# Kernel optimization log

Measured on AMD Instinct MI355X. Metric: run time of the kernel, lower is better.

The kernel has to match this reference:

```python
import jax, jax.numpy as jnp
import numpy as np

NUM_LAYERS = 12
D = 256          # d_model
H = 8            # n_head
DK = D // H      # qk_dim = v_dim = 32
FFD = 1024       # ffd_dim
B, L = 32, 448
EPS = 1e-6
MAXLEN = 500


def _sinusoidal_pos_emb(maxlen, hidden_dim):
    depth = hidden_dim / 2
    positions = np.arange(maxlen, dtype=np.float32)[:, None]
    depths = np.arange(depth, dtype=np.float32)[None, :] / depth
    angle_rads = positions * (1.0 / np.power(10000.0, depths))
    pe = np.concatenate([np.sin(angle_rads), np.cos(angle_rads)], axis=-1)
    return jnp.asarray(pe, jnp.float32)


def setup_inputs() -> dict:
    key = jax.random.key(0)
    ks = jax.random.split(key, 16)
    s = 0.02
    inp = {
        "x": jax.random.normal(ks[0], (B, L, D), jnp.float32),
        "mask": jnp.zeros((B, L), jnp.bool_),
        "pos_emb": _sinusoidal_pos_emb(MAXLEN - 1, D)[:L],  # [L, D]
        "Wq": jax.random.normal(ks[1], (NUM_LAYERS, D, D), jnp.float32) * s,
        "bq": jnp.zeros((NUM_LAYERS, D), jnp.float32),
        "Wk": jax.random.normal(ks[2], (NUM_LAYERS, D, D), jnp.float32) * s,
        "bk": jnp.zeros((NUM_LAYERS, D), jnp.float32),
        "Wv": jax.random.normal(ks[3], (NUM_LAYERS, D, D), jnp.float32) * s,
        "bv": jnp.zeros((NUM_LAYERS, D), jnp.float32),
        "Wo": jax.random.normal(ks[4], (NUM_LAYERS, D, D), jnp.float32) * s,
        "bo": jnp.zeros((NUM_LAYERS, D), jnp.float32),
        "W1": jax.random.normal(ks[5], (NUM_LAYERS, D, FFD), jnp.float32) * s,
        "bf1": jnp.zeros((NUM_LAYERS, FFD), jnp.float32),
        "W2": jax.random.normal(ks[6], (NUM_LAYERS, FFD, D), jnp.float32) * s,
        "bf2": jnp.zeros((NUM_LAYERS, D), jnp.float32),
        "ln1_g": jnp.ones((NUM_LAYERS, D), jnp.float32),
        "ln1_b": jnp.zeros((NUM_LAYERS, D), jnp.float32),
        "ln2_g": jnp.ones((NUM_LAYERS, D), jnp.float32),
        "ln2_b": jnp.zeros((NUM_LAYERS, D), jnp.float32),
    }
    return inp


def _layer_norm(x, g, b):
    mu = jnp.mean(x, axis=-1, keepdims=True)
    var = jnp.mean(jnp.square(x - mu), axis=-1, keepdims=True)
    return (x - mu) * jax.lax.rsqrt(var + EPS) * g + b


def _encoder_forward(x, mask, pos_emb, Wq, bq, Wk, bk, Wv, bv, Wo, bo,
                     W1, bf1, W2, bf2, ln1_g, ln1_b, ln2_g, ln2_b):
    Bx, Lx, _ = x.shape
    scale = 1.0 / np.sqrt(DK)
    x = x + pos_emb[None, :Lx, :]
    mask_b = mask[:, None, None, :]  # [B,1,1,L], True = masked
    for i in range(NUM_LAYERS):
        # --- pre-norm attention ---
        nx = _layer_norm(x, ln1_g[i], ln1_b[i])
        q = (nx @ Wq[i] + bq[i]).reshape(Bx, Lx, H, DK)
        k = (nx @ Wk[i] + bk[i]).reshape(Bx, Lx, H, DK)
        v = (nx @ Wv[i] + bv[i]).reshape(Bx, Lx, H, DK)
        dot = jnp.einsum("bihd,bjhd->bhij", q, k) * scale
        dot = jnp.where(mask_b, -10000.0, dot)
        attn = jax.nn.softmax(dot, axis=-1)
        o = jnp.einsum("bhij,bjhd->bihd", attn, v).reshape(Bx, Lx, D)
        x = x + (o @ Wo[i] + bo[i])
        # --- pre-norm FFN (exact GELU, as torch nn.GELU) ---
        nx2 = _layer_norm(x, ln2_g[i], ln2_b[i])
        h = jax.nn.gelu(nx2 @ W1[i] + bf1[i], approximate=False)
        x = x + (h @ W2[i] + bf2[i])
    return x


def reference(x, mask, pos_emb, Wq, bq, Wk, bk, Wv, bv, Wo, bo,
              W1, bf1, W2, bf2, ln1_g, ln1_b, ln2_g, ln2_b):
    return _encoder_forward(x, mask, pos_emb, Wq, bq, Wk, bk, Wv, bv, Wo, bo,
                            W1, bf1, W2, bf2, ln1_g, ln1_b, ln2_g, ln2_b)
```

## Files before the change

kernel.cpp:

```cpp
#include <hip/hip_runtime.h>

#define NL 12
#define DM 256
#define FFDIM 1024
#define BBATCH 32
#define LSEQ 448
#define MTOK (BBATCH*LSEQ)
#define EPSF 1e-6f
#define QSCALE_LOG2E (0.17677669529663687f * 1.4426950408889634f)

typedef __attribute__((ext_vector_type(8))) short bf16x8;
typedef __attribute__((ext_vector_type(4))) float f32x4;
typedef unsigned short u16;
typedef unsigned int u32;

__device__ __forceinline__ u16 f2bf(float f) {
    union { float f; u32 u; } v; v.f = f;
    u32 r = v.u + 0x7fffu + ((v.u >> 16) & 1u);
    return (u16)(r >> 16);
}
__device__ __forceinline__ float gelu_exact(float x) {
    return 0.5f * x * (1.0f + erff(x * 0.70710678118654752f));
}
__device__ __forceinline__ void gload16(const u16* g, u16* l) {
    __builtin_amdgcn_global_load_lds(
        (const __attribute__((address_space(1))) u32*)g,
        (__attribute__((address_space(3))) u32*)l, 16, 0, 0);
}

__global__ __launch_bounds__(256) void add_pos_k(
    const float* __restrict__ x, const float* __restrict__ pe, float* __restrict__ out)
{
    int i = blockIdx.x * 256 + threadIdx.x;
    float4 xv = ((const float4*)x)[i];
    float4 pv = ((const float4*)pe)[i % (LSEQ * DM / 4)];
    float4 r;
    r.x = xv.x + pv.x; r.y = xv.y + pv.y; r.z = xv.z + pv.z; r.w = xv.w + pv.w;
    ((float4*)out)[i] = r;
}

__global__ __launch_bounds__(256) void ln_k(
    const float* __restrict__ x, const float* __restrict__ g,
    const float* __restrict__ b, u16* __restrict__ out)
{
    const int w = threadIdx.x >> 6, lane = threadIdx.x & 63;
    const int row = blockIdx.x * 4 + w;
    float4 v = ((const float4*)(x + (size_t)row * DM))[lane];
    float s = v.x + v.y + v.z + v.w;
#pragma unroll
    for (int off = 32; off; off >>= 1) s += __shfl_xor(s, off);
    float mu = s * (1.0f / 256.0f);
    float d0 = v.x - mu, d1 = v.y - mu, d2 = v.z - mu, d3 = v.w - mu;
    float sq = d0*d0 + d1*d1 + d2*d2 + d3*d3;
#pragma unroll
    for (int off = 32; off; off >>= 1) sq += __shfl_xor(sq, off);
    float rs = rsqrtf(sq * (1.0f / 256.0f) + EPSF);
    float4 gv = ((const float4*)g)[lane];
    float4 bv = ((const float4*)b)[lane];
    ushort4 o;
    o.x = f2bf(d0 * rs * gv.x + bv.x);
    o.y = f2bf(d1 * rs * gv.y + bv.y);
    o.z = f2bf(d2 * rs * gv.z + bv.z);
    o.w = f2bf(d3 * rs * gv.w + bv.w);
    *(ushort4*)(out + (size_t)row * DM + lane * 4) = o;
}

__global__ __launch_bounds__(256) void twt_k(
    const float* __restrict__ in, u16* __restrict__ out,
    int K, int N, int in_lstride, int out_lstride)
{
    __shared__ float tl[32][33];
    const int l = blockIdx.z;
    const int n0 = blockIdx.x * 32, k0 = blockIdx.y * 32;
    const int tx = threadIdx.x & 31, ty = threadIdx.x >> 5;
    const float* src = in + (size_t)l * in_lstride;
#pragma unroll
    for (int i = 0; i < 4; ++i)
        tl[ty + 8*i][tx] = src[(size_t)(k0 + ty + 8*i) * N + n0 + tx];
    __syncthreads();
    u16* dst = out + (size_t)l * out_lstride;
#pragma unroll
    for (int i = 0; i < 4; ++i)
        dst[(size_t)(n0 + ty + 8*i) * K + k0 + tx] = f2bf(tl[tx][ty + 8*i]);
}

__global__ __launch_bounds__(256) void pack_bias_k(
    const float* __restrict__ bq, const float* __restrict__ bk,
    const float* __restrict__ bv, float* __restrict__ bqkv)
{
    int i = blockIdx.x * 256 + threadIdx.x;
    if (i >= NL * 768) return;
    int l = i / 768, c = i % 768;
    float v = (c < 256) ? bq[l*256 + c] : (c < 512) ? bk[l*256 + c - 256] : bv[l*256 + c - 512];
    bqkv[i] = v;
}

template<int BN, int EPI>
__global__ __launch_bounds__(256, (BN == 64) ? 4 : 3) void mm_k(
    const u16* __restrict__ A, int lda, const u16* __restrict__ Bt,
    const float* __restrict__ bias, void* __restrict__ C, int ldc, int K,
    u16* __restrict__ vtg)
{
    __shared__ u16 As[2][128 * 32];
    __shared__ u16 Bs[2][BN * 32];
    constexpr int MT = BN / 32;
    const int tid = threadIdx.x;
    const int by = blockIdx.x, bx = blockIdx.y;
    const int w = tid >> 6, lane = tid & 63;
    const int lm = lane & 15, lk = lane >> 4;
    const int m0 = (BN == 128) ? ((w >> 1) * 64) : (w * 32);
    const int n0 = (BN == 128) ? ((w & 1) * 64) : 0;
    const int lrow = lane >> 2, lcol = (lane & 3) * 8;

    const u16* Ab = A + (size_t)(by * 128) * lda;
    const u16* Bb = Bt + (size_t)(bx * BN) * K;

    f32x4 zz = {0.f, 0.f, 0.f, 0.f};
    f32x4 acc[MT][4];
#pragma unroll
    for (int i = 0; i < MT; ++i)
#pragma unroll
        for (int j = 0; j < 4; ++j) acc[i][j] = zz;

    auto stage = [&](int buf, int k0) {
#pragma unroll
        for (int i = 0; i < 2; ++i) {
            int seg = w * 2 + i;
            gload16(Ab + (size_t)(seg * 16 + lrow) * lda + k0 + lcol, &As[buf][seg * 512]);
        }
        if constexpr (BN == 128) {
#pragma unroll
            for (int i = 0; i < 2; ++i) {
                int seg = w * 2 + i;
                gload16(Bb + (size_t)(seg * 16 + lrow) * K + k0 + lcol, &Bs[buf][seg * 512]);
            }
        } else {
            gload16(Bb + (size_t)(w * 16 + lrow) * K + k0 + lcol, &Bs[buf][w * 512]);
        }
    };

    stage(0, 0);
    const int NK = K >> 5;
    for (int it = 0; it < NK; ++it) {
        const int cur = it & 1;
        __syncthreads();
        if (it + 1 < NK) stage(1 - cur, (it + 1) * 32);
        bf16x8 af[MT], bfr[4];
#pragma unroll
        for (int mt = 0; mt < MT; ++mt)
            af[mt] = *(const bf16x8*)&As[cur][(m0 + mt*16 + lm)*32 + lk*8];
#pragma unroll
        for (int nt = 0; nt < 4; ++nt)
            bfr[nt] = *(const bf16x8*)&Bs[cur][(n0 + nt*16 + lm)*32 + lk*8];
#pragma unroll
        for (int mt = 0; mt < MT; ++mt)
#pragma unroll
            for (int nt = 0; nt < 4; ++nt)
                acc[mt][nt] = __builtin_amdgcn_mfma_f32_16x16x32_bf16(af[mt], bfr[nt], acc[mt][nt], 0, 0, 0);
    }

    float bv[4];
#pragma unroll
    for (int nt = 0; nt < 4; ++nt) bv[nt] = bias[bx*BN + n0 + nt*16 + lm];
#pragma unroll
    for (int mt = 0; mt < MT; ++mt) {
        int grow0 = by*128 + m0 + mt*16 + lk*4;
#pragma unroll
        for (int nt = 0; nt < 4; ++nt) {
            int gcol = bx*BN + n0 + nt*16 + lm;
            float v0 = acc[mt][nt][0] + bv[nt];
            float v1 = acc[mt][nt][1] + bv[nt];
            float v2 = acc[mt][nt][2] + bv[nt];
            float v3 = acc[mt][nt][3] + bv[nt];
            if constexpr (EPI == 1) {
                u16* cp = (u16*)C + (size_t)grow0 * ldc + gcol;
                cp[0]            = f2bf(gelu_exact(v0));
                cp[ldc]          = f2bf(gelu_exact(v1));
                cp[2*(size_t)ldc] = f2bf(gelu_exact(v2));
                cp[3*(size_t)ldc] = f2bf(gelu_exact(v3));
            } else if constexpr (EPI == 3) {
                if (gcol < 512) {
                    float qs = (gcol < 256) ? QSCALE_LOG2E : 1.0f;
                    u16* cp = (u16*)C + (size_t)grow0 * ldc + gcol;
                    cp[0]            = f2bf(v0 * qs);
                    cp[ldc]          = f2bf(v1 * qs);
                    cp[2*(size_t)ldc] = f2bf(v2 * qs);
                    cp[3*(size_t)ldc] = f2bf(v3 * qs);
                } else {
                    int c = gcol - 512;
                    int hh = c >> 5, d = c & 31;
                    u32 bidx = (u32)grow0 / 448u;
                    int srow = grow0 - (int)bidx * 448;
                    ushort4 st;
                    st.x = f2bf(v0); st.y = f2bf(v1); st.z = f2bf(v2); st.w = f2bf(v3);
                    *(ushort4*)&vtg[((size_t)(bidx*8 + hh)*32 + d)*448 + srow] = st;
                }
            } else {
                float* p = (float*)C + (size_t)grow0 * ldc + gcol;
                p[0]   += v0;
                p[ldc] += v1;
                p[2*(size_t)ldc] += v2;
                p[3*(size_t)ldc] += v3;
            }
        }
    }
}

__global__ __launch_bounds__(256, 4) void attn_k(
    const u16* __restrict__ qkv, const u16* __restrict__ vtg,
    const unsigned char* __restrict__ mask, u16* __restrict__ ob)
{
    __shared__ u16 Klds[448 * 32];
    __shared__ u16 Plds[4][16 * 68];
    const int tid = threadIdx.x, w = tid >> 6, lane = tid & 63;
    const int lm = lane & 15, lk = lane >> 4;
    const int bid = blockIdx.x;
    const int bh = bid & 255, sg = bid >> 8;
    const int b = bh >> 3, h = bh & 7;
    const size_t rowbase = (size_t)b * LSEQ;

#pragma unroll
    for (int i = 0; i < 7; ++i) {
        int seg = w * 7 + i;
        gload16(qkv + (rowbase + seg * 16 + (lane >> 2)) * 768 + 256 + h * 32 + (lane & 3) * 8,
                &Klds[seg * 512]);
    }
    unsigned mbits = 0;
#pragma unroll
    for (int t = 0; t < 28; ++t)
        mbits |= (mask[b * LSEQ + t * 16 + lm] ? 1u : 0u) << t;
    __syncthreads();

    const u16* Vb = vtg + (size_t)bh * 32 * 448;
    f32x4 zz = {0.f, 0.f, 0.f, 0.f};

    const int q0 = (sg * 4 + w) * 16;
    bf16x8 qf = *(const bf16x8*)(qkv + (rowbase + q0 + lm) * 768 + h * 32 + lk * 8);

    f32x4 oacc[2] = {zz, zz};
    float sum[4] = {0.f, 0.f, 0.f, 0.f};
    u16* P = &Plds[w][0];
#pragma unroll
    for (int cc = 0; cc < 7; ++cc) {
#pragma unroll
        for (int tt = 0; tt < 4; ++tt) {
            int t = cc*4 + tt;
            bf16x8 kf = *(const bf16x8*)&Klds[(t*16 + lm)*32 + lk*8];
            f32x4 s = __builtin_amdgcn_mfma_f32_16x16x32_bf16(qf, kf, zz, 0, 0, 0);
            bool m = (mbits >> t) & 1;
#pragma unroll
            for (int r = 0; r < 4; ++r) {
                float e = m ? 0.f : exp2f(s[r]);
                sum[r] += e;
                P[(lk*4 + r)*68 + tt*16 + lm] = f2bf(e);
            }
        }
        bf16x8 pa0 = *(const bf16x8*)&P[lm*68 + lk*8];
        bf16x8 pa1 = *(const bf16x8*)&P[lm*68 + 32 + lk*8];
#pragma unroll
        for (int dt = 0; dt < 2; ++dt) {
            bf16x8 vb0 = *(const bf16x8*)(Vb + (size_t)(dt*16 + lm)*448 + cc*64 + lk*8);
            bf16x8 vb1 = *(const bf16x8*)(Vb + (size_t)(dt*16 + lm)*448 + cc*64 + 32 + lk*8);
            oacc[dt] = __builtin_amdgcn_mfma_f32_16x16x32_bf16(pa0, vb0, oacc[dt], 0, 0, 0);
            oacc[dt] = __builtin_amdgcn_mfma_f32_16x16x32_bf16(pa1, vb1, oacc[dt], 0, 0, 0);
        }
    }
#pragma unroll
    for (int off = 1; off < 16; off <<= 1)
#pragma unroll
        for (int r = 0; r < 4; ++r) sum[r] += __shfl_xor(sum[r], off);
    float inv[4];
#pragma unroll
    for (int r = 0; r < 4; ++r) inv[r] = 1.0f / sum[r];

#pragma unroll
    for (int dt = 0; dt < 2; ++dt)
#pragma unroll
        for (int r = 0; r < 4; ++r)
            ob[(rowbase + q0 + lk*4 + r)*256 + h*32 + dt*16 + lm] = f2bf(oacc[dt][r] * inv[r]);
}

extern "C" void kernel_launch(void* const* d_in, const int* in_sizes, int n_in,
                              void* d_out, int out_size, void* d_ws, size_t ws_size,
                              hipStream_t stream)
{
    const float* x_in = (const float*)d_in[0];
    const unsigned char* mask = (const unsigned char*)d_in[1];
    const float* pe   = (const float*)d_in[2];
    const float* Wq = (const float*)d_in[3];
    const float* bq = (const float*)d_in[4];
    const float* Wk = (const float*)d_in[5];
    const float* bk = (const float*)d_in[6];
    const float* Wv = (const float*)d_in[7];
    const float* bv = (const float*)d_in[8];
    const float* Wo = (const float*)d_in[9];
    const float* bo = (const float*)d_in[10];
    const float* W1 = (const float*)d_in[11];
    const float* bf1 = (const float*)d_in[12];
    const float* W2 = (const float*)d_in[13];
    const float* bf2 = (const float*)d_in[14];
    const float* ln1_g = (const float*)d_in[15];
    const float* ln1_b = (const float*)d_in[16];
    const float* ln2_g = (const float*)d_in[17];
    const float* ln2_b = (const float*)d_in[18];

    float* x = (float*)d_out;
    u16* ws = (u16*)d_ws;
    u16* nx   = ws;
    u16* qkv  = nx + 3670016;
    u16* ob   = qkv + 11010048;
    u16* vtg  = ob + 3670016;
    u16* hb   = qkv;
    u16* wqkvt = vtg + 3670016;
    u16* wot  = wqkvt + 2359296;
    u16* w1t  = wot + 786432;
    u16* w2t  = w1t + 3145728;
    float* bqkv = (float*)(w2t + 3145728);

    add_pos_k<<<MTOK * DM / 1024, 256, 0, stream>>>(x_in, pe, x);

    twt_k<<<dim3(8, 8, NL), 256, 0, stream>>>(Wq, wqkvt,          256, 256, 65536, 196608);
    twt_k<<<dim3(8, 8, NL), 256, 0, stream>>>(Wk, wqkvt + 65536,  256, 256, 65536, 196608);
    twt_k<<<dim3(8, 8, NL), 256, 0, stream>>>(Wv, wqkvt + 131072, 256, 256, 65536, 196608);
    twt_k<<<dim3(8, 8, NL), 256, 0, stream>>>(Wo, wot, 256, 256, 65536, 65536);
    twt_k<<<dim3(32, 8, NL), 256, 0, stream>>>(W1, w1t, 256, 1024, 262144, 262144);
    twt_k<<<dim3(8, 32, NL), 256, 0, stream>>>(W2, w2t, 1024, 256, 262144, 262144);
    pack_bias_k<<<(NL * 768 + 255) / 256, 256, 0, stream>>>(bq, bk, bv, bqkv);

    for (int l = 0; l < NL; ++l) {
        ln_k<<<MTOK / 4, 256, 0, stream>>>(x, ln1_g + l*256, ln1_b + l*256, nx);
        mm_k<128, 3><<<dim3(112, 6), 256, 0, stream>>>(
            nx, 256, wqkvt + (size_t)l*196608, bqkv + l*768, qkv, 768, 256, vtg);
        attn_k<<<1792, 256, 0, stream>>>(qkv, vtg, mask, ob);
        mm_k<64, 2><<<dim3(112, 4), 256, 0, stream>>>(
            ob, 256, wot + (size_t)l*65536, bo + l*256, x, 256, 256, nullptr);
        ln_k<<<MTOK / 4, 256, 0, stream>>>(x, ln2_g + l*256, ln2_b + l*256, nx);
        mm_k<128, 1><<<dim3(112, 8), 256, 0, stream>>>(
            nx, 256, w1t + (size_t)l*262144, bf1 + l*1024, hb, 1024, 256, nullptr);
        mm_k<64, 2><<<dim3(112, 4), 256, 0, stream>>>(
            hb, 1024, w2t + (size_t)l*262144, bf2 + l*256, x, 256, 1024, nullptr);
    }
}
```

Measured before the change: 1.541 ms.

## Fuse residual add and LayerNorm into full-row output-projection GEMM epilogues

```diff
diff --git a/kernel.cpp b/kernel.cpp
--- a/kernel.cpp
+++ b/kernel.cpp
@@ -28,24 +28,18 @@
         (__attribute__((address_space(3))) u32*)l, 16, 0, 0);
 }
 
-__global__ __launch_bounds__(256) void add_pos_k(
-    const float* __restrict__ x, const float* __restrict__ pe, float* __restrict__ out)
-{
-    int i = blockIdx.x * 256 + threadIdx.x;
-    float4 xv = ((const float4*)x)[i];
-    float4 pv = ((const float4*)pe)[i % (LSEQ * DM / 4)];
-    float4 r;
-    r.x = xv.x + pv.x; r.y = xv.y + pv.y; r.z = xv.z + pv.z; r.w = xv.w + pv.w;
-    ((float4*)out)[i] = r;
-}
-
-__global__ __launch_bounds__(256) void ln_k(
-    const float* __restrict__ x, const float* __restrict__ g,
-    const float* __restrict__ b, u16* __restrict__ out)
+__global__ __launch_bounds__(256) void ln0_k(
+    const float* __restrict__ xin, const float* __restrict__ pe,
+    const float* __restrict__ g, const float* __restrict__ b,
+    float* __restrict__ x, u16* __restrict__ nx)
 {
     const int w = threadIdx.x >> 6, lane = threadIdx.x & 63;
     const int row = blockIdx.x * 4 + w;
-    float4 v = ((const float4*)(x + (size_t)row * DM))[lane];
+    const int prow = row % LSEQ;
+    float4 v = ((const float4*)(xin + (size_t)row * DM))[lane];
+    float4 p = ((const float4*)(pe + (size_t)prow * DM))[lane];
+    v.x += p.x; v.y += p.y; v.z += p.z; v.w += p.w;
+    ((float4*)(x + (size_t)row * DM))[lane] = v;
     float s = v.x + v.y + v.z + v.w;
 #pragma unroll
     for (int off = 32; off; off >>= 1) s += __shfl_xor(s, off);
@@ -62,7 +56,7 @@
     o.y = f2bf(d1 * rs * gv.y + bv.y);
     o.z = f2bf(d2 * rs * gv.z + bv.z);
     o.w = f2bf(d3 * rs * gv.w + bv.w);
-    *(ushort4*)(out + (size_t)row * DM + lane * 4) = o;
+    *(ushort4*)(nx + (size_t)row * DM + lane * 4) = o;
 }
 
 __global__ __launch_bounds__(256) void twt_k(
@@ -95,95 +89,86 @@
     bqkv[i] = v;
 }
 
-template<int BN, int EPI>
-__global__ __launch_bounds__(256, (BN == 64) ? 4 : 3) void mm_k(
+template<int EPI>
+__global__ __launch_bounds__(256, 3) void mm_k(
     const u16* __restrict__ A, int lda, const u16* __restrict__ Bt,
-    const float* __restrict__ bias, void* __restrict__ C, int ldc, int K,
+    const float* __restrict__ bias, u16* __restrict__ C, int ldc, int K,
     u16* __restrict__ vtg)
 {
     __shared__ u16 As[2][128 * 32];
-    __shared__ u16 Bs[2][BN * 32];
-    constexpr int MT = BN / 32;
+    __shared__ u16 Bs[2][128 * 32];
     const int tid = threadIdx.x;
     const int by = blockIdx.x, bx = blockIdx.y;
     const int w = tid >> 6, lane = tid & 63;
     const int lm = lane & 15, lk = lane >> 4;
-    const int m0 = (BN == 128) ? ((w >> 1) * 64) : (w * 32);
-    const int n0 = (BN == 128) ? ((w & 1) * 64) : 0;
+    const int m0 = (w >> 1) * 64, n0 = (w & 1) * 64;
     const int lrow = lane >> 2, lcol = (lane & 3) * 8;
 
     const u16* Ab = A + (size_t)(by * 128) * lda;
-    const u16* Bb = Bt + (size_t)(bx * BN) * K;
+    const u16* Bb = Bt + (size_t)(bx * 128) * K;
 
     f32x4 zz = {0.f, 0.f, 0.f, 0.f};
-    f32x4 acc[MT][4];
-#pragma unroll
-    for (int i = 0; i < MT; ++i)
+    f32x4 acc[4][4];
+#pragma unroll
+    for (int i = 0; i < 4; ++i)
 #pragma unroll
         for (int j = 0; j < 4; ++j) acc[i][j] = zz;
 
-    auto stage = [&](int buf, int k0) {
-#pragma unroll
-        for (int i = 0; i < 2; ++i) {
-            int seg = w * 2 + i;
-            gload16(Ab + (size_t)(seg * 16 + lrow) * lda + k0 + lcol, &As[buf][seg * 512]);
-        }
-        if constexpr (BN == 128) {
+    for (int k0 = 0; k0 < K; k0 += 64) {
+        __syncthreads();
+#pragma unroll
+        for (int p = 0; p < 2; ++p)
 #pragma unroll
             for (int i = 0; i < 2; ++i) {
                 int seg = w * 2 + i;
-                gload16(Bb + (size_t)(seg * 16 + lrow) * K + k0 + lcol, &Bs[buf][seg * 512]);
-            }
-        } else {
-            gload16(Bb + (size_t)(w * 16 + lrow) * K + k0 + lcol, &Bs[buf][w * 512]);
-        }
-    };
-
-    stage(0, 0);
-    const int NK = K >> 5;
-    for (int it = 0; it < NK; ++it) {
-        const int cur = it & 1;
+                gload16(Ab + (size_t)(seg * 16 + lrow) * lda + k0 + p * 32 + lcol,
+                        &As[p][seg * 512]);
+                gload16(Bb + (size_t)(seg * 16 + lrow) * K + k0 + p * 32 + lcol,
+                        &Bs[p][seg * 512]);
+            }
         __syncthreads();
-        if (it + 1 < NK) stage(1 - cur, (it + 1) * 32);
-        bf16x8 af[MT], bfr[4];
-#pragma unroll
-        for (int mt = 0; mt < MT; ++mt)
-            af[mt] = *(const bf16x8*)&As[cur][(m0 + mt*16 + lm)*32 + lk*8];
-#pragma unroll
-        for (int nt = 0; nt < 4; ++nt)
-            bfr[nt] = *(const bf16x8*)&Bs[cur][(n0 + nt*16 + lm)*32 + lk*8];
-#pragma unroll
-        for (int mt = 0; mt < MT; ++mt)
+#pragma unroll
+        for (int p = 0; p < 2; ++p) {
+            bf16x8 af[4], bfr[4];
+#pragma unroll
+            for (int mt = 0; mt < 4; ++mt)
+                af[mt] = *(const bf16x8*)&As[p][(m0 + mt*16 + lm)*32 + lk*8];
 #pragma unroll
             for (int nt = 0; nt < 4; ++nt)
-                acc[mt][nt] = __builtin_amdgcn_mfma_f32_16x16x32_bf16(af[mt], bfr[nt], acc[mt][nt], 0, 0, 0);
+                bfr[nt] = *(const bf16x8*)&Bs[p][(n0 + nt*16 + lm)*32 + lk*8];
+#pragma unroll
+            for (int mt = 0; mt < 4; ++mt)
+#pragma unroll
+                for (int nt = 0; nt < 4; ++nt)
+                    acc[mt][nt] = __builtin_amdgcn_mfma_f32_16x16x32_bf16(af[mt], bfr[nt], acc[mt][nt], 0, 0, 0);
+        }
     }
 
     float bv[4];
 #pragma unroll
-    for (int nt = 0; nt < 4; ++nt) bv[nt] = bias[bx*BN + n0 + nt*16 + lm];
-#pragma unroll
-    for (int mt = 0; mt < MT; ++mt) {
+    for (int nt = 0; nt < 4; ++nt) bv[nt] = bias[bx*128 + n0 + nt*16 + lm];
+#pragma unroll
+    for (int mt = 0; mt < 4; ++mt) {
         int grow0 = by*128 + m0 + mt*16 + lk*4;
 #pragma unroll
         for (int nt = 0; nt < 4; ++nt) {
-            int gcol = bx*BN + n0 + nt*16 + lm;
+            int gcol = bx*128 + n0 + nt*16 + lm;
             float v0 = acc[mt][nt][0] + bv[nt];
             float v1 = acc[mt][nt][1] + bv[nt];
             float v2 = acc[mt][nt][2] + bv[nt];
             float v3 = acc[mt][nt][3] + bv[nt];
             if constexpr (EPI == 1) {
-                u16* cp = (u16*)C + (size_t)grow0 * ldc + gcol;
-                cp[0]            = f2bf(gelu_exact(v0));
-                cp[ldc]          = f2bf(gelu_exact(v1));
+                u16* cp = C + (size_t)grow0 * ldc + gcol;
+                cp[0]             = f2bf(gelu_exact(v0));
+                cp[ldc]           = f2bf(gelu_exact(v1));
                 cp[2*(size_t)ldc] = f2bf(gelu_exact(v2));
                 cp[3*(size_t)ldc] = f2bf(gelu_exact(v3));
-            } else if constexpr (EPI == 3) {
+            } else {
                 if (gcol < 512) {
                     float qs = (gcol < 256) ? QSCALE_LOG2E : 1.0f;
-                    u16* cp = (u16*)C + (size_t)grow0 * ldc + gcol;
-                    cp[0]            = f2bf(v0 * qs);
-                    cp[ldc]          = f2bf(v1 * qs);
+                    u16* cp = C + (size_t)grow0 * ldc + gcol;
+                    cp[0]             = f2bf(v0 * qs);
+                    cp[ldc]           = f2bf(v1 * qs);
                     cp[2*(size_t)ldc] = f2bf(v2 * qs);
                     cp[3*(size_t)ldc] = f2bf(v3 * qs);
                 } else {
@@ -195,13 +180,111 @@
                     st.x = f2bf(v0); st.y = f2bf(v1); st.z = f2bf(v2); st.w = f2bf(v3);
                     *(ushort4*)&vtg[((size_t)(bidx*8 + hh)*32 + d)*448 + srow] = st;
                 }
-            } else {
-                float* p = (float*)C + (size_t)grow0 * ldc + gcol;
-                p[0]   += v0;
-                p[ldc] += v1;
-                p[2*(size_t)ldc] += v2;
-                p[3*(size_t)ldc] += v3;
-            }
+            }
+        }
+    }
+}
+
+template<bool DOLN>
+__global__ __launch_bounds__(256, 3) void mmrow_k(
+    const u16* __restrict__ A, int lda, const u16* __restrict__ Bt,
+    const float* __restrict__ bias, float* __restrict__ X,
+    const float* __restrict__ g, const float* __restrict__ b,
+    u16* __restrict__ nx, int K)
+{
+    __shared__ u16 As[2][64 * 32];
+    __shared__ u16 Bs[2][256 * 32];
+    const int tid = threadIdx.x, by = blockIdx.x;
+    const int w = tid >> 6, lane = tid & 63;
+    const int lm = lane & 15, lk = lane >> 4;
+    const int m0 = w * 16;
+    const int lrow = lane >> 2, lcol = (lane & 3) * 8;
+
+    const u16* Ab = A + (size_t)(by * 64) * lda;
+
+    f32x4 zz = {0.f, 0.f, 0.f, 0.f};
+    f32x4 acc[16];
+#pragma unroll
+    for (int i = 0; i < 16; ++i) acc[i] = zz;
+
+    for (int k0 = 0; k0 < K; k0 += 64) {
+        __syncthreads();
+#pragma unroll
+        for (int p = 0; p < 2; ++p) {
+            gload16(Ab + (size_t)(w * 16 + lrow) * lda + k0 + p * 32 + lcol,
+                    &As[p][w * 512]);
+#pragma unroll
+            for (int i = 0; i < 4; ++i) {
+                int seg = w * 4 + i;
+                gload16(Bt + (size_t)(seg * 16 + lrow) * K + k0 + p * 32 + lcol,
+                        &Bs[p][seg * 512]);
+            }
+        }
+        __syncthreads();
+#pragma unroll
+        for (int p = 0; p < 2; ++p) {
+            bf16x8 af = *(const bf16x8*)&As[p][(m0 + lm)*32 + lk*8];
+#pragma unroll
+            for (int nt = 0; nt < 16; ++nt) {
+                bf16x8 bfr = *(const bf16x8*)&Bs[p][(nt*16 + lm)*32 + lk*8];
+                acc[nt] = __builtin_amdgcn_mfma_f32_16x16x32_bf16(af, bfr, acc[nt], 0, 0, 0);
+            }
+        }
+    }
+
+    const int row0 = by*64 + m0 + lk*4;
+    float sum[4] = {0.f, 0.f, 0.f, 0.f};
+#pragma unroll
+    for (int nt = 0; nt < 16; ++nt) {
+        float bvv = bias[nt*16 + lm];
+        const float* xp = X + (size_t)row0 * 256 + nt*16 + lm;
+#pragma unroll
+        for (int r = 0; r < 4; ++r) {
+            float xn = xp[(size_t)r * 256] + acc[nt][r] + bvv;
+            acc[nt][r] = xn;
+            sum[r] += xn;
+        }
+    }
+    if constexpr (DOLN) {
+#pragma unroll
+        for (int off = 1; off < 16; off <<= 1)
+#pragma unroll
+            for (int r = 0; r < 4; ++r) sum[r] += __shfl_xor(sum[r], off);
+        float mu[4], sq[4] = {0.f, 0.f, 0.f, 0.f};
+#pragma unroll
+        for (int r = 0; r < 4; ++r) mu[r] = sum[r] * (1.0f / 256.0f);
+#pragma unroll
+        for (int nt = 0; nt < 16; ++nt)
+#pragma unroll
+            for (int r = 0; r < 4; ++r) {
+                float d = acc[nt][r] - mu[r];
+                sq[r] += d * d;
+            }
+#pragma unroll
+        for (int off = 1; off < 16; off <<= 1)
+#pragma unroll
+            for (int r = 0; r < 4; ++r) sq[r] += __shfl_xor(sq[r], off);
+        float rs[4];
+#pragma unroll
+        for (int r = 0; r < 4; ++r) rs[r] = rsqrtf(sq[r] * (1.0f / 256.0f) + EPSF);
+#pragma unroll
+        for (int nt = 0; nt < 16; ++nt) {
+            int col = nt*16 + lm;
+            float gc = g[col], bc = b[col];
+            float* xp = X + (size_t)row0 * 256 + col;
+            u16* np = nx + (size_t)row0 * 256 + col;
+#pragma unroll
+            for (int r = 0; r < 4; ++r) {
+                xp[(size_t)r * 256] = acc[nt][r];
+                np[(size_t)r * 256] = f2bf((acc[nt][r] - mu[r]) * rs[r] * gc + bc);
+            }
+        }
+    } else {
+#pragma unroll
+        for (int nt = 0; nt < 16; ++nt) {
+            float* xp = X + (size_t)row0 * 256 + nt*16 + lm;
+#pragma unroll
+            for (int r = 0; r < 4; ++r) xp[(size_t)r * 256] = acc[nt][r];
         }
     }
 }
@@ -317,8 +400,6 @@
     u16* w2t  = w1t + 3145728;
     float* bqkv = (float*)(w2t + 3145728);
 
-    add_pos_k<<<MTOK * DM / 1024, 256, 0, stream>>>(x_in, pe, x);
-
     twt_k<<<dim3(8, 8, NL), 256, 0, stream>>>(Wq, wqkvt,          256, 256, 65536, 196608);
     twt_k<<<dim3(8, 8, NL), 256, 0, stream>>>(Wk, wqkvt + 65536,  256, 256, 65536, 196608);
     twt_k<<<dim3(8, 8, NL), 256, 0, stream>>>(Wv, wqkvt + 131072, 256, 256, 65536, 196608);
@@ -327,17 +408,25 @@
     twt_k<<<dim3(8, 32, NL), 256, 0, stream>>>(W2, w2t, 1024, 256, 262144, 262144);
     pack_bias_k<<<(NL * 768 + 255) / 256, 256, 0, stream>>>(bq, bk, bv, bqkv);
 
+    ln0_k<<<MTOK / 4, 256, 0, stream>>>(x_in, pe, ln1_g, ln1_b, x, nx);
+
     for (int l = 0; l < NL; ++l) {
-        ln_k<<<MTOK / 4, 256, 0, stream>>>(x, ln1_g + l*256, ln1_b + l*256, nx);
-        mm_k<128, 3><<<dim3(112, 6), 256, 0, stream>>>(
+        mm_k<3><<<dim3(112, 6), 256, 0, stream>>>(
             nx, 256, wqkvt + (size_t)l*196608, bqkv + l*768, qkv, 768, 256, vtg);
         attn_k<<<1792, 256, 0, stream>>>(qkv, vtg, mask, ob);
-        mm_k<64, 2><<<dim3(112, 4), 256, 0, stream>>>(
-            ob, 256, wot + (size_t)l*65536, bo + l*256, x, 256, 256, nullptr);
-        ln_k<<<MTOK / 4, 256, 0, stream>>>(x, ln2_g + l*256, ln2_b + l*256, nx);
-        mm_k<128, 1><<<dim3(112, 8), 256, 0, stream>>>(
+        mmrow_k<true><<<224, 256, 0, stream>>>(
+            ob, 256, wot + (size_t)l*65536, bo + l*256, x,
+            ln2_g + l*256, ln2_b + l*256, nx, 256);
+        mm_k<1><<<dim3(112, 8), 256, 0, stream>>>(
             nx, 256, w1t + (size_t)l*262144, bf1 + l*1024, hb, 1024, 256, nullptr);
-        mm_k<64, 2><<<dim3(112, 4), 256, 0, stream>>>(
-            hb, 1024, w2t + (size_t)l*262144, bf2 + l*256, x, 256, 1024, nullptr);
-    }
-}
+        if (l < NL - 1) {
+            mmrow_k<true><<<224, 256, 0, stream>>>(
+                hb, 1024, w2t + (size_t)l*262144, bf2 + l*256, x,
+                ln1_g + (l+1)*256, ln1_b + (l+1)*256, nx, 1024);
+        } else {
+            mmrow_k<false><<<224, 256, 0, stream>>>(
+                hb, 1024, w2t + (size_t)l*262144, bf2 + l*256, x,
+                nullptr, nullptr, nullptr, 1024);
+        }
+    }
+}
```

After: 1.456 ms. 1.06x faster.
